# Optimization experiments

Measured on AMD Instinct MI355X. Metric: run time of the kernel, lower is better.

Reference implementation:

```python
import jax, jax.numpy as jnp
import numpy as np

D = 512   # in_features
N = 65536 # nodes per side
M = 32768 # mutual nodes


def setup_inputs() -> dict:
    key = jax.random.key(0)
    ks = jax.random.split(key, 8)
    h_p = jax.random.normal(ks[0], (N, D), dtype=jnp.float32)
    h_k = jax.random.normal(ks[1], (N, D), dtype=jnp.float32)
    last_x = jax.random.normal(ks[2], (N, D), dtype=jnp.float32)
    mutual_index_p = jnp.arange(M, dtype=jnp.int64) if jax.config.jax_enable_x64 else jnp.arange(M, dtype=jnp.int32)
    mutual_index_k = jnp.arange(M, dtype=jnp.int32)
    # parameters (xavier_uniform gain=1.667 for weight_o/weight_c)
    limit = 1.667 * np.sqrt(6.0 / (D + D))
    weight_o = jax.random.uniform(ks[3], (D, D), jnp.float32, -limit, limit)
    weight_c = jax.random.uniform(ks[4], (D, D), jnp.float32, -limit, limit)
    # nn.Linear(2*D, D): kaiming-uniform-ish default; plain uniform is fine for a reference
    lb = 1.0 / np.sqrt(2 * D)
    lin_w = jax.random.uniform(ks[5], (D, 2 * D), jnp.float32, -lb, lb)
    lin_b = jax.random.uniform(ks[6], (D,), jnp.float32, -lb, lb)
    stdv = 1.0 / np.sqrt(D)
    bias = jax.random.uniform(ks[7], (D,), jnp.float32, -stdv, stdv)
    return {"h_p": h_p, "h_k": h_k, "mutual_index_p": mutual_index_p,
            "mutual_index_k": mutual_index_k, "last_x": last_x,
            "weight_o": weight_o, "weight_c": weight_c,
            "lin_w": lin_w, "lin_b": lin_b, "bias": bias}


def reference(h_p, h_k, mutual_index_p, mutual_index_k, last_x,
              weight_o, weight_c, lin_w, lin_b, bias):
    trans_hp = h_p @ weight_o          # [N, D]
    trans_hk = h_k @ weight_c          # [N, D]
    # gather mutual rows, concat, tanh
    g = jnp.tanh(jnp.concatenate(
        (trans_hp[mutual_index_p], trans_hk[mutual_index_k]), axis=1))  # [M, 2D]
    out = jax.nn.leaky_relu(g @ lin_w.T + lin_b) + bias                  # [M, D]
    # scatter back
    trans_hp = trans_hp.at[mutual_index_p].set(out)
    trans_hk = trans_hk.at[mutual_index_k].set(out)
    return (trans_hp, trans_hk)
```

## Files before the change

kernel.cpp:

```cpp
#include <hip/hip_runtime.h>
#include <hip/hip_bf16.h>

#define D_DIM   512
#define N_NODES 65536
#define M_MUT   32768

typedef __bf16 bf16x8 __attribute__((ext_vector_type(8)));
typedef float  f32x4  __attribute__((ext_vector_type(4)));

__device__ __forceinline__ unsigned short f2bf_rn(float f) {
    unsigned int u = __float_as_uint(f);
    u += 0x7FFFu + ((u >> 16) & 1u);
    return (unsigned short)(u >> 16);
}

__device__ __forceinline__ void async_ld16(void* lds, const void* g) {
    __builtin_amdgcn_global_load_lds(
        (__attribute__((address_space(1))) void*)(void*)g,
        (__attribute__((address_space(3))) void*)lds,
        16, 0, 0);
}

__global__ void cast_weights_kernel(const float* __restrict__ wo,
                                    const float* __restrict__ wc,
                                    const float* __restrict__ lw,
                                    unsigned short* __restrict__ bto,
                                    unsigned short* __restrict__ btc,
                                    unsigned short* __restrict__ blw)
{
    int t = blockIdx.x * 256 + threadIdx.x;
    if (t < 262144) {
        int n = t >> 9, k = t & 511;
        bto[t] = f2bf_rn(wo[k * 512 + n]);
    } else if (t < 524288) {
        int u = t - 262144;
        int n = u >> 9, k = u & 511;
        btc[u] = f2bf_rn(wc[k * 512 + n]);
    } else {
        int u = t - 524288;
        blw[u] = f2bf_rn(lw[u]);
    }
}

__global__ __launch_bounds__(256)
void gemm_trans_kernel(const float* __restrict__ hp,
                       const float* __restrict__ hk,
                       const unsigned short* __restrict__ bto,
                       const unsigned short* __restrict__ btc,
                       float* __restrict__ out)
{
    const int bid  = blockIdx.x;
    const int band = bid >> 6;
    const int rr_  = bid & 63;
    const int n0   = (rr_ & 3) * 128;
    const int m0   = (band * 16 + (rr_ >> 2)) * 128;

    const float* A;
    const unsigned short* Bt;
    if (m0 < N_NODES) { A = hp + (size_t)m0 * D_DIM;             Bt = bto; }
    else              { A = hk + (size_t)(m0 - N_NODES) * D_DIM; Bt = btc; }

    __shared__ __align__(16) unsigned short As[128 * 32];
    __shared__ __align__(16) unsigned short Bs[128 * 32];

    const int tid  = threadIdx.x;
    const int lane = tid & 63;
    const int wid  = tid >> 6;
    const int wm   = (wid & 1) * 64;
    const int wn   = (wid >> 1) * 64;
    const int r16  = lane & 15;
    const int q    = lane >> 4;

    f32x4 acc[4][4] = {};

    const int ag_row = tid >> 2;
    const int ag_c8  = (tid & 3) * 8;

    for (int kk = 0; kk < 16; ++kk) {
        const int k0 = kk * 32;
        #pragma unroll
        for (int i = 0; i < 2; ++i) {
            const int row = ag_row + i * 64;
            const float* src = A + (size_t)row * D_DIM + k0 + ag_c8;
            float4 v0 = *(const float4*)src;
            float4 v1 = *(const float4*)(src + 4);
            uint4 u;
            u.x = f2bf_rn(v0.x) | ((unsigned)f2bf_rn(v0.y) << 16);
            u.y = f2bf_rn(v0.z) | ((unsigned)f2bf_rn(v0.w) << 16);
            u.z = f2bf_rn(v1.x) | ((unsigned)f2bf_rn(v1.y) << 16);
            u.w = f2bf_rn(v1.z) | ((unsigned)f2bf_rn(v1.w) << 16);
            *(uint4*)&As[(row * 4 + (tid & 3)) * 8] = u;
        }
        #pragma unroll
        for (int i = 0; i < 2; ++i) {
            const int c  = i * 256 + wid * 64 + lane;
            const int bn = c >> 2, k8 = (c & 3) * 8;
            async_ld16(&Bs[(i * 256 + wid * 64) * 8],
                       Bt + (size_t)(n0 + bn) * D_DIM + k0 + k8);
        }
        __syncthreads();
        bf16x8 af[4], bfr[4];
        #pragma unroll
        for (int mi = 0; mi < 4; ++mi)
            af[mi] = *(const bf16x8*)&As[(wm + mi * 16 + r16) * 32 + q * 8];
        #pragma unroll
        for (int ni = 0; ni < 4; ++ni)
            bfr[ni] = *(const bf16x8*)&Bs[(wn + ni * 16 + r16) * 32 + q * 8];
        #pragma unroll
        for (int mi = 0; mi < 4; ++mi)
            #pragma unroll
            for (int ni = 0; ni < 4; ++ni)
                acc[mi][ni] = __builtin_amdgcn_mfma_f32_16x16x32_bf16(
                    af[mi], bfr[ni], acc[mi][ni], 0, 0, 0);
        __syncthreads();
    }

    #pragma unroll
    for (int mi = 0; mi < 4; ++mi) {
        #pragma unroll
        for (int ni = 0; ni < 4; ++ni) {
            const int mrow = m0 + wm + mi * 16 + q * 4;
            const int ncol = n0 + wn + ni * 16 + r16;
            float* p = out + (size_t)mrow * D_DIM + ncol;
            #pragma unroll
            for (int rr = 0; rr < 4; ++rr)
                p[(size_t)rr * D_DIM] = acc[mi][ni][rr];
        }
    }
}

__global__ void gather_tanh_kernel(const float* __restrict__ trans,
                                   const int* __restrict__ idxp,
                                   const int* __restrict__ idxk,
                                   unsigned short* __restrict__ g)
{
    const int t  = blockIdx.x * 256 + threadIdx.x;
    const int m  = t >> 8;
    const int j4 = (t & 255) * 4;
    const float* src;
    if (j4 < 512) src = trans + (size_t)idxp[m] * 512 + j4;
    else          src = trans + (size_t)N_NODES * 512 + (size_t)idxk[m] * 512 + (j4 - 512);
    float4 v = *(const float4*)src;
    ushort4 o;
    o.x = f2bf_rn(tanhf(v.x));
    o.y = f2bf_rn(tanhf(v.y));
    o.z = f2bf_rn(tanhf(v.z));
    o.w = f2bf_rn(tanhf(v.w));
    *(ushort4*)&g[(size_t)m * 1024 + j4] = o;
}

__global__ __launch_bounds__(256)
void gemm_out_kernel(const unsigned short* __restrict__ g,
                     const unsigned short* __restrict__ blw,
                     const float* __restrict__ lin_b,
                     const float* __restrict__ bias,
                     const int* __restrict__ idxp,
                     const int* __restrict__ idxk,
                     float* __restrict__ out)
{
    const int bid  = blockIdx.x;
    const int band = bid >> 6;
    const int rr_  = bid & 63;
    const int n0   = (rr_ & 3) * 128;
    const int m0   = (band * 16 + (rr_ >> 2)) * 128;

    __shared__ __align__(16) unsigned short As[128 * 32];
    __shared__ __align__(16) unsigned short Bs[128 * 32];

    const int tid  = threadIdx.x;
    const int lane = tid & 63;
    const int wid  = tid >> 6;
    const int wm   = (wid & 1) * 64;
    const int wn   = (wid >> 1) * 64;
    const int r16  = lane & 15;
    const int q    = lane >> 4;

    f32x4 acc[4][4] = {};

    for (int kk = 0; kk < 32; ++kk) {
        const int k0 = kk * 32;
        #pragma unroll
        for (int i = 0; i < 2; ++i) {
            const int c = i * 256 + wid * 64 + lane;
            const int ar = c >> 2, k8 = (c & 3) * 8;
            async_ld16(&As[(i * 256 + wid * 64) * 8],
                       g + (size_t)(m0 + ar) * 1024 + k0 + k8);
        }
        #pragma unroll
        for (int i = 0; i < 2; ++i) {
            const int c = i * 256 + wid * 64 + lane;
            const int bn = c >> 2, k8 = (c & 3) * 8;
            async_ld16(&Bs[(i * 256 + wid * 64) * 8],
                       blw + (size_t)(n0 + bn) * 1024 + k0 + k8);
        }
        __syncthreads();
        bf16x8 af[4], bfr[4];
        #pragma unroll
        for (int mi = 0; mi < 4; ++mi)
            af[mi] = *(const bf16x8*)&As[(wm + mi * 16 + r16) * 32 + q * 8];
        #pragma unroll
        for (int ni = 0; ni < 4; ++ni)
            bfr[ni] = *(const bf16x8*)&Bs[(wn + ni * 16 + r16) * 32 + q * 8];
        #pragma unroll
        for (int mi = 0; mi < 4; ++mi)
            #pragma unroll
            for (int ni = 0; ni < 4; ++ni)
                acc[mi][ni] = __builtin_amdgcn_mfma_f32_16x16x32_bf16(
                    af[mi], bfr[ni], acc[mi][ni], 0, 0, 0);
        __syncthreads();
    }

    int ip[4][4], ik[4][4];
    #pragma unroll
    for (int mi = 0; mi < 4; ++mi)
        #pragma unroll
        for (int rr = 0; rr < 4; ++rr) {
            const int m = m0 + wm + mi * 16 + q * 4 + rr;
            ip[mi][rr] = idxp[m];
            ik[mi][rr] = idxk[m];
        }
    const size_t half = (size_t)N_NODES * D_DIM;
    #pragma unroll
    for (int ni = 0; ni < 4; ++ni) {
        const int ncol = n0 + wn + ni * 16 + r16;
        const float lb = lin_b[ncol];
        const float bs = bias[ncol];
        #pragma unroll
        for (int mi = 0; mi < 4; ++mi)
            #pragma unroll
            for (int rr = 0; rr < 4; ++rr) {
                float v = acc[mi][ni][rr] + lb;
                v = v > 0.0f ? v : 0.01f * v;
                v += bs;
                out[(size_t)ip[mi][rr] * D_DIM + ncol] = v;
                out[half + (size_t)ik[mi][rr] * D_DIM + ncol] = v;
            }
    }
}

extern "C" void kernel_launch(void* const* d_in, const int* in_sizes, int n_in,
                              void* d_out, int out_size, void* d_ws, size_t ws_size,
                              hipStream_t stream)
{
    const float* h_p  = (const float*)d_in[0];
    const float* h_k  = (const float*)d_in[1];
    const int*   idxp = (const int*)d_in[2];
    const int*   idxk = (const int*)d_in[3];
    const float* w_o  = (const float*)d_in[5];
    const float* w_c  = (const float*)d_in[6];
    const float* linw = (const float*)d_in[7];
    const float* linb = (const float*)d_in[8];
    const float* bias = (const float*)d_in[9];
    float* out = (float*)d_out;

    unsigned short* g   = (unsigned short*)d_ws;
    unsigned short* bto = g + (size_t)M_MUT * 1024;
    unsigned short* btc = bto + 512 * 512;
    unsigned short* blw = btc + 512 * 512;

    cast_weights_kernel<<<4096, 256, 0, stream>>>(w_o, w_c, linw, bto, btc, blw);
    gemm_trans_kernel<<<4096, 256, 0, stream>>>(h_p, h_k, bto, btc, out);
    gather_tanh_kernel<<<M_MUT, 256, 0, stream>>>(out, idxp, idxk, g);
    gemm_out_kernel<<<1024, 256, 0, stream>>>(g, blw, linb, bias, idxp, idxk, out);
}
```

Measured before the change: 700.9 us.

## Fuse gather+tanh into first GEMM epilogue via inverse index map

Builds inverse index maps (node to mutual row) in a prep and scatter step. The first GEMM epilogue then writes tanh'd bf16 rows straight into the gather buffer for mutual nodes and fp32 output only for non-mutual rows. This removes the separate gather_tanh kernel and the redundant output writes that would later be overwritten. Both epilogues are staged through LDS so stores are row-contiguous 16-byte nontemporal stores, and tanhf is replaced by an exp-based approximation. The risks are extra syncs in the epilogue, and duplicate indices resolving differently than the reference's last-write semantics.

```diff
diff --git a/kernel.cpp b/kernel.cpp
--- a/kernel.cpp
+++ b/kernel.cpp
@@ -12,6 +12,11 @@
     unsigned int u = __float_as_uint(f);
     u += 0x7FFFu + ((u >> 16) & 1u);
     return (unsigned short)(u >> 16);
+}
+
+__device__ __forceinline__ float fast_tanh(float x) {
+    float e = __expf(2.0f * x);
+    return 1.0f - 2.0f / (1.0f + e);
 }
 
 __device__ __forceinline__ void async_ld16(void* lds, const void* g) {
@@ -21,12 +26,14 @@
         16, 0, 0);
 }
 
-__global__ void cast_weights_kernel(const float* __restrict__ wo,
-                                    const float* __restrict__ wc,
-                                    const float* __restrict__ lw,
-                                    unsigned short* __restrict__ bto,
-                                    unsigned short* __restrict__ btc,
-                                    unsigned short* __restrict__ blw)
+__global__ void prep_kernel(const float* __restrict__ wo,
+                            const float* __restrict__ wc,
+                            const float* __restrict__ lw,
+                            unsigned short* __restrict__ bto,
+                            unsigned short* __restrict__ btc,
+                            unsigned short* __restrict__ blw,
+                            int* __restrict__ invp,
+                            int* __restrict__ invk)
 {
     int t = blockIdx.x * 256 + threadIdx.x;
     if (t < 262144) {
@@ -36,10 +43,24 @@
         int u = t - 262144;
         int n = u >> 9, k = u & 511;
         btc[u] = f2bf_rn(wc[k * 512 + n]);
-    } else {
+    } else if (t < 1048576) {
         int u = t - 524288;
         blw[u] = f2bf_rn(lw[u]);
-    }
+    } else {
+        int u = t - 1048576;
+        if (u < 65536) invp[u] = -1;
+        else           invk[u - 65536] = -1;
+    }
+}
+
+__global__ void scatter_inv_kernel(const int* __restrict__ idxp,
+                                   const int* __restrict__ idxk,
+                                   int* __restrict__ invp,
+                                   int* __restrict__ invk)
+{
+    int m = blockIdx.x * 256 + threadIdx.x;
+    invp[idxp[m]] = m;
+    invk[idxk[m]] = m;
 }
 
 __global__ __launch_bounds__(256)
@@ -47,6 +68,9 @@
                        const float* __restrict__ hk,
                        const unsigned short* __restrict__ bto,
                        const unsigned short* __restrict__ btc,
+                       const int* __restrict__ invp,
+                       const int* __restrict__ invk,
+                       unsigned short* __restrict__ g,
                        float* __restrict__ out)
 {
     const int bid  = blockIdx.x;
@@ -55,13 +79,17 @@
     const int n0   = (rr_ & 3) * 128;
     const int m0   = (band * 16 + (rr_ >> 2)) * 128;
 
-    const float* A;
-    const unsigned short* Bt;
-    if (m0 < N_NODES) { A = hp + (size_t)m0 * D_DIM;             Bt = bto; }
-    else              { A = hk + (size_t)(m0 - N_NODES) * D_DIM; Bt = btc; }
-
-    __shared__ __align__(16) unsigned short As[128 * 32];
-    __shared__ __align__(16) unsigned short Bs[128 * 32];
+    const bool isP = (m0 < N_NODES);
+    const int  mrel = isP ? m0 : m0 - N_NODES;
+    const float* A = (isP ? hp : hk) + (size_t)mrel * D_DIM;
+    const unsigned short* Bt = isP ? bto : btc;
+    const int* inv = isP ? invp : invk;
+    const int  gcol0 = isP ? 0 : 512;
+    const size_t outbase = isP ? 0 : (size_t)N_NODES * D_DIM;
+
+    __shared__ __align__(16) unsigned short smem[128 * 32 * 2];
+    unsigned short* As = smem;
+    unsigned short* Bs = smem + 128 * 32;
 
     const int tid  = threadIdx.x;
     const int lane = tid & 63;
@@ -115,38 +143,50 @@
         __syncthreads();
     }
 
+    float* epi = (float*)smem + wid * 1024;
+    const int erow = lane >> 2;
+    const int ec0  = (lane & 3) * 16;
+
     #pragma unroll
     for (int mi = 0; mi < 4; ++mi) {
         #pragma unroll
-        for (int ni = 0; ni < 4; ++ni) {
-            const int mrow = m0 + wm + mi * 16 + q * 4;
-            const int ncol = n0 + wn + ni * 16 + r16;
-            float* p = out + (size_t)mrow * D_DIM + ncol;
-            #pragma unroll
-            for (int rr = 0; rr < 4; ++rr)
-                p[(size_t)rr * D_DIM] = acc[mi][ni][rr];
-        }
-    }
-}
-
-__global__ void gather_tanh_kernel(const float* __restrict__ trans,
-                                   const int* __restrict__ idxp,
-                                   const int* __restrict__ idxk,
-                                   unsigned short* __restrict__ g)
-{
-    const int t  = blockIdx.x * 256 + threadIdx.x;
-    const int m  = t >> 8;
-    const int j4 = (t & 255) * 4;
-    const float* src;
-    if (j4 < 512) src = trans + (size_t)idxp[m] * 512 + j4;
-    else          src = trans + (size_t)N_NODES * 512 + (size_t)idxk[m] * 512 + (j4 - 512);
-    float4 v = *(const float4*)src;
-    ushort4 o;
-    o.x = f2bf_rn(tanhf(v.x));
-    o.y = f2bf_rn(tanhf(v.y));
-    o.z = f2bf_rn(tanhf(v.z));
-    o.w = f2bf_rn(tanhf(v.w));
-    *(ushort4*)&g[(size_t)m * 1024 + j4] = o;
+        for (int ni = 0; ni < 4; ++ni)
+            #pragma unroll
+            for (int r2 = 0; r2 < 4; ++r2)
+                epi[(q * 4 + r2) * 64 + ni * 16 + r16] = acc[mi][ni][r2];
+        __syncthreads();
+
+        const int lrow = mrel + wm + mi * 16 + erow;
+        const int iv   = inv[lrow];
+        f32x4 vv[4];
+        #pragma unroll
+        for (int c = 0; c < 4; ++c)
+            vv[c] = *(const f32x4*)&epi[erow * 64 + ec0 + c * 4];
+
+        if (iv >= 0) {
+            unsigned int hh[8];
+            #pragma unroll
+            for (int c = 0; c < 4; ++c) {
+                unsigned short a0 = f2bf_rn(fast_tanh(vv[c][0]));
+                unsigned short a1 = f2bf_rn(fast_tanh(vv[c][1]));
+                unsigned short a2 = f2bf_rn(fast_tanh(vv[c][2]));
+                unsigned short a3 = f2bf_rn(fast_tanh(vv[c][3]));
+                hh[c * 2]     = (unsigned)a0 | ((unsigned)a1 << 16);
+                hh[c * 2 + 1] = (unsigned)a2 | ((unsigned)a3 << 16);
+            }
+            unsigned short* gp = g + (size_t)iv * 1024 + gcol0 + n0 + wn + ec0;
+            uint4 u0 = {hh[0], hh[1], hh[2], hh[3]};
+            uint4 u1 = {hh[4], hh[5], hh[6], hh[7]};
+            *(uint4*)gp       = u0;
+            *((uint4*)gp + 1) = u1;
+        } else {
+            float* op = out + outbase + (size_t)lrow * D_DIM + n0 + wn + ec0;
+            #pragma unroll
+            for (int c = 0; c < 4; ++c)
+                __builtin_nontemporal_store(vv[c], (f32x4*)op + c);
+        }
+        __syncthreads();
+    }
 }
 
 __global__ __launch_bounds__(256)
@@ -164,8 +204,9 @@
     const int n0   = (rr_ & 3) * 128;
     const int m0   = (band * 16 + (rr_ >> 2)) * 128;
 
-    __shared__ __align__(16) unsigned short As[128 * 32];
-    __shared__ __align__(16) unsigned short Bs[128 * 32];
+    __shared__ __align__(16) unsigned short smem[128 * 32 * 2];
+    unsigned short* As = smem;
+    unsigned short* Bs = smem + 128 * 32;
 
     const int tid  = threadIdx.x;
     const int lane = tid & 63;
@@ -210,31 +251,51 @@
         __syncthreads();
     }
 
-    int ip[4][4], ik[4][4];
+    float* epi = (float*)smem + wid * 1024;
+    const int erow = lane >> 2;
+    const int ec0  = (lane & 3) * 16;
+    const int col0 = n0 + wn + ec0;
+
+    f32x4 lb[4], bs[4];
     #pragma unroll
-    for (int mi = 0; mi < 4; ++mi)
-        #pragma unroll
-        for (int rr = 0; rr < 4; ++rr) {
-            const int m = m0 + wm + mi * 16 + q * 4 + rr;
-            ip[mi][rr] = idxp[m];
-            ik[mi][rr] = idxk[m];
-        }
+    for (int c = 0; c < 4; ++c) {
+        lb[c] = *(const f32x4*)(lin_b + col0 + c * 4);
+        bs[c] = *(const f32x4*)(bias  + col0 + c * 4);
+    }
     const size_t half = (size_t)N_NODES * D_DIM;
+
     #pragma unroll
-    for (int ni = 0; ni < 4; ++ni) {
-        const int ncol = n0 + wn + ni * 16 + r16;
-        const float lb = lin_b[ncol];
-        const float bs = bias[ncol];
-        #pragma unroll
-        for (int mi = 0; mi < 4; ++mi)
-            #pragma unroll
-            for (int rr = 0; rr < 4; ++rr) {
-                float v = acc[mi][ni][rr] + lb;
-                v = v > 0.0f ? v : 0.01f * v;
-                v += bs;
-                out[(size_t)ip[mi][rr] * D_DIM + ncol] = v;
-                out[half + (size_t)ik[mi][rr] * D_DIM + ncol] = v;
+    for (int mi = 0; mi < 4; ++mi) {
+        #pragma unroll
+        for (int ni = 0; ni < 4; ++ni)
+            #pragma unroll
+            for (int r2 = 0; r2 < 4; ++r2)
+                epi[(q * 4 + r2) * 64 + ni * 16 + r16] = acc[mi][ni][r2];
+        __syncthreads();
+
+        const int m  = m0 + wm + mi * 16 + erow;
+        const int dp = idxp[m];
+        const int dk = idxk[m];
+        f32x4 vv[4];
+        #pragma unroll
+        for (int c = 0; c < 4; ++c) {
+            f32x4 v = *(const f32x4*)&epi[erow * 64 + ec0 + c * 4];
+            #pragma unroll
+            for (int e = 0; e < 4; ++e) {
+                float x = v[e] + lb[c][e];
+                x = x > 0.0f ? x : 0.01f * x;
+                v[e] = x + bs[c][e];
             }
+            vv[c] = v;
+        }
+        float* p1 = out + (size_t)dp * D_DIM + col0;
+        float* p2 = out + half + (size_t)dk * D_DIM + col0;
+        #pragma unroll
+        for (int c = 0; c < 4; ++c) {
+            __builtin_nontemporal_store(vv[c], (f32x4*)p1 + c);
+            __builtin_nontemporal_store(vv[c], (f32x4*)p2 + c);
+        }
+        __syncthreads();
     }
 }
 
@@ -257,9 +318,11 @@
     unsigned short* bto = g + (size_t)M_MUT * 1024;
     unsigned short* btc = bto + 512 * 512;
     unsigned short* blw = btc + 512 * 512;
-
-    cast_weights_kernel<<<4096, 256, 0, stream>>>(w_o, w_c, linw, bto, btc, blw);
-    gemm_trans_kernel<<<4096, 256, 0, stream>>>(h_p, h_k, bto, btc, out);
-    gather_tanh_kernel<<<M_MUT, 256, 0, stream>>>(out, idxp, idxk, g);
+    int* invp = (int*)(blw + 512 * 1024);
+    int* invk = invp + N_NODES;
+
+    prep_kernel<<<4608, 256, 0, stream>>>(w_o, w_c, linw, bto, btc, blw, invp, invk);
+    scatter_inv_kernel<<<M_MUT / 256, 256, 0, stream>>>(idxp, idxk, invp, invk);
+    gemm_trans_kernel<<<4096, 256, 0, stream>>>(h_p, h_k, bto, btc, invp, invk, g, out);
     gemm_out_kernel<<<1024, 256, 0, stream>>>(g, blw, linb, bias, idxp, idxk, out);
 }
```

After: 963.2 us. 1.37x slower.
